# Optimization experiments

Measured on AMD Instinct MI355X. Metric: run time of the kernel, lower is better.

Reference implementation:

```python
import jax, jax.numpy as jnp
import numpy as np

DIM = 384
DSTATE = 16
DTRANK = 24  # ceil(384/16)
DCONV = 3
F = 3  # fixed segment factor from rearrange 'b (f t) c'


def setup_inputs() -> dict:
    key = jax.random.key(0)
    ks = jax.random.split(key, 8)
    d_in = DIM // 2
    x = jax.random.normal(ks[0], (4, 6144, DIM), dtype=jnp.float32)
    in_proj_w = jax.random.normal(ks[1], (DIM, DIM), dtype=jnp.float32) * 0.05
    in_proj_b = jnp.zeros((DIM,), jnp.float32)
    conv_w = jax.random.normal(ks[2], (d_in, 2, DCONV), dtype=jnp.float32) * 0.3
    conv_b = jnp.zeros((d_in,), jnp.float32)
    A = jnp.tile(jnp.arange(1, DSTATE + 1, dtype=jnp.float32)[None, :], (d_in, 1))
    A_log = jnp.log(A)
    Ab_log = jnp.log(A)
    D = jnp.ones((d_in,), jnp.float32)
    x_proj_w = jax.random.normal(ks[3], (DTRANK + 2 * DSTATE, d_in), dtype=jnp.float32) * 0.05
    dt_init_std = DTRANK ** (-0.5)
    dt_proj_w = jax.random.uniform(ks[4], (d_in, DTRANK), minval=-dt_init_std, maxval=dt_init_std, dtype=jnp.float32)
    dt = jnp.exp(jax.random.uniform(ks[5], (d_in,), dtype=jnp.float32) * (np.log(0.1) - np.log(0.001)) + np.log(0.001))
    dt = jnp.clip(dt, 1e-4)
    dt_proj_b = dt + jnp.log(-jnp.expm1(-dt))
    out_proj_w = jax.random.normal(ks[6], (DIM, DIM), dtype=jnp.float32) * 0.05
    out_proj_b = jnp.zeros((DIM,), jnp.float32)
    return dict(x=x, in_proj_w=in_proj_w, in_proj_b=in_proj_b, conv_w=conv_w, conv_b=conv_b,
                A_log=A_log, Ab_log=Ab_log, D=D, x_proj_w=x_proj_w, dt_proj_w=dt_proj_w,
                dt_proj_b=dt_proj_b, out_proj_w=out_proj_w, out_proj_b=out_proj_b)


def _ssm(u, Amat, x_proj_w, dt_proj_w, dt_proj_b, Dvec):
    # u: (b, d, l) selective scan (no z-gating; z handled outside by concat)
    x_dbl = jnp.einsum('rd,bdl->brl', x_proj_w, u)
    dt = x_dbl[:, :DTRANK]                      # (b, r, l)
    Bm = x_dbl[:, DTRANK:DTRANK + DSTATE]       # (b, n, l)
    Cm = x_dbl[:, DTRANK + DSTATE:]             # (b, n, l)
    delta = jax.nn.softplus(jnp.einsum('dr,brl->bdl', dt_proj_w, dt) + dt_proj_b[None, :, None])
    dA = jnp.exp(jnp.einsum('bdl,dn->lbdn', delta, Amat))      # (l, b, d, n)
    dBu = jnp.einsum('bdl,bnl->lbdn', delta * u, Bm)           # (l, b, d, n)
    Ct = jnp.transpose(Cm, (2, 0, 1))                          # (l, b, n)
    h0 = jnp.zeros(u.shape[:2] + (DSTATE,), u.dtype)

    def step(h, inp):
        dA_t, dBu_t, C_t = inp
        h = dA_t * h + dBu_t
        return h, jnp.einsum('bdn,bn->bd', h, C_t)

    _, ys = jax.lax.scan(step, h0, (dA, dBu, Ct))
    return jnp.transpose(ys, (1, 2, 0)) + u * Dvec[None, :, None]


def reference(x, in_proj_w, in_proj_b, conv_w, conv_b, A_log, Ab_log, D,
              x_proj_w, dt_proj_w, dt_proj_b, out_proj_w, out_proj_b):
    b, seqlen, dim = x.shape
    t = seqlen // F
    xp = (x @ in_proj_w.T + in_proj_b).reshape(b * F, t, dim)
    xp = jnp.transpose(xp, (0, 2, 1))  # (bf, dim, t)
    xc = jax.lax.conv_general_dilated(xp, conv_w, (1,), 'SAME',
                                      dimension_numbers=('NCH', 'OIH', 'NCH'),
                                      feature_group_count=dim // 2)
    xc = jax.nn.silu(xc + conv_b[None, :, None])  # (bf, dim//2, t)
    z = xc
    A = -jnp.exp(A_log)
    Ab = -jnp.exp(Ab_log)
    fwd = _ssm(xc, A, x_proj_w, dt_proj_w, dt_proj_b, D)
    bwd = jnp.flip(_ssm(jnp.flip(xc, -1), Ab, x_proj_w, dt_proj_w, dt_proj_b, D), -1)
    y = jnp.concatenate([fwd + bwd, z], axis=1)   # (bf, dim, t)
    y = jnp.transpose(y, (0, 2, 1))
    out = y @ out_proj_w.T + out_proj_b
    return out.reshape(b, seqlen, dim)
```

## Files before the change

### kernel.cpp

```cpp
#include <hip/hip_runtime.h>
#include <hip/hip_bf16.h>
#include <math.h>

#define NSQ   12
#define LQ    2048
#define DIMQ  384
#define DIQ   192
#define RKQ   24
#define NCHK  16
#define CLEN  128

#define BM 128
#define BN 64
#define BK 64

typedef unsigned short u16;
typedef __attribute__((ext_vector_type(8))) short s16x8;
typedef __attribute__((ext_vector_type(4))) float f32x4;
typedef __attribute__((ext_vector_type(4))) unsigned short u16x4;
typedef __attribute__((ext_vector_type(8))) unsigned short u16x8;

__device__ __forceinline__ float siluf(float x) {
  return x / (1.0f + __expf(-x));
}
__device__ __forceinline__ float softplusf(float x) {
  return (x > 20.0f) ? x : log1pf(expf(x));
}
__device__ __forceinline__ u16 f2bf(float f) {
  unsigned int u = __float_as_uint(f);
  u += 0x7FFFu + ((u >> 16) & 1u);
  return (u16)(u >> 16);
}
__device__ __forceinline__ float bf2f(u16 h) {
  return __uint_as_float(((unsigned int)h) << 16);
}

union F4 { float4 v; float a[4]; };

template<int CTRL>
__device__ __forceinline__ float dpp_add(float x) {
  union { float f; int i; } u, r;
  u.f = x;
  r.i = __builtin_amdgcn_update_dpp(0, u.i, CTRL, 0xF, 0xF, true);
  return x + r.f;
}

__global__ void k_prep(const float* __restrict__ xpw, const float* __restrict__ dtw,
                       const float* __restrict__ inw, const float* __restrict__ outw,
                       u16* __restrict__ winb, u16* __restrict__ woutb,
                       u16* __restrict__ wc_hi, u16* __restrict__ wc_lo) {
  int t = threadIdx.x + blockIdx.x * blockDim.x;
  int stride = blockDim.x * gridDim.x;
  for (int i = t; i < DIMQ * DIMQ; i += stride) {
    winb[i]  = f2bf(inw[i]);
    woutb[i] = f2bf(outw[i]);
  }
  for (int i = t; i < 224 * 192; i += stride) {
    const int r = i / 192, k = i % 192;
    float v;
    if (r < 192) {
      float s = 0.0f;
      for (int q = 0; q < RKQ; ++q) s = fmaf(dtw[r * RKQ + q], xpw[q * 192 + k], s);
      v = s;
    } else {
      v = xpw[(24 + (r - 192)) * 192 + k];
    }
    const u16 hi = f2bf(v);
    wc_hi[i] = hi;
    wc_lo[i] = f2bf(v - bf2f(hi));
  }
}

__launch_bounds__(256)
__global__ void k_inproj(const float* __restrict__ x, const u16* __restrict__ wbf,
                         const float* __restrict__ bias, float* __restrict__ xp_t) {
  __shared__ __align__(16) char smem[33792];
  u16 (*As)[72] = (u16(*)[72])smem;
  u16 (*Bs)[72] = (u16(*)[72])(smem + 18432);
  const int t = threadIdx.x;
  const int m0 = blockIdx.x * BM;
  const int n0 = blockIdx.y * BN;
  const int lane = t & 63, wid = t >> 6;
  const int wm = wid >> 1, wn = wid & 1;
  const int lr = lane & 15, lg = lane >> 4;
  f32x4 acc[4][2];
#pragma unroll
  for (int i = 0; i < 4; ++i)
#pragma unroll
    for (int j = 0; j < 2; ++j) acc[i][j] = (f32x4){0.f, 0.f, 0.f, 0.f};

  for (int k0 = 0; k0 < 384; k0 += BK) {
    float4 a_ld[8];
#pragma unroll
    for (int i = 0; i < 8; ++i) {
      const int idx = t + i * 256;
      const int row = idx >> 4, kq = (idx & 15) * 4;
      a_ld[i] = *(const float4*)&x[(size_t)(m0 + row) * 384 + k0 + kq];
    }
    u16x8 b_ld[2];
#pragma unroll
    for (int i = 0; i < 2; ++i) {
      const int idx = t + i * 256;
      const int n = idx >> 3, kq = (idx & 7) * 8;
      b_ld[i] = *(const u16x8*)&wbf[(size_t)(n0 + n) * 384 + k0 + kq];
    }
    __syncthreads();
#pragma unroll
    for (int i = 0; i < 8; ++i) {
      const int idx = t + i * 256;
      const int row = idx >> 4, kq = (idx & 15) * 4;
      u16x4 p;
      p.x = f2bf(a_ld[i].x); p.y = f2bf(a_ld[i].y);
      p.z = f2bf(a_ld[i].z); p.w = f2bf(a_ld[i].w);
      *(u16x4*)&As[row][kq] = p;
    }
#pragma unroll
    for (int i = 0; i < 2; ++i) {
      const int idx = t + i * 256;
      const int n = idx >> 3, kq = (idx & 7) * 8;
      *(u16x8*)&Bs[n][kq] = b_ld[i];
    }
    __syncthreads();
#pragma unroll
    for (int kh = 0; kh < BK; kh += 32) {
      s16x8 af[4], bf[2];
#pragma unroll
      for (int mi = 0; mi < 4; ++mi)
        af[mi] = *(const s16x8*)&As[wm * 64 + mi * 16 + lr][kh + lg * 8];
#pragma unroll
      for (int ni = 0; ni < 2; ++ni)
        bf[ni] = *(const s16x8*)&Bs[wn * 32 + ni * 16 + lr][kh + lg * 8];
#pragma unroll
      for (int mi = 0; mi < 4; ++mi)
#pragma unroll
        for (int ni = 0; ni < 2; ++ni)
          acc[mi][ni] = __builtin_amdgcn_mfma_f32_16x16x32_bf16(af[mi], bf[ni], acc[mi][ni], 0, 0, 0);
    }
    __syncthreads();
  }
  float (*T)[132] = (float(*)[132])smem;
#pragma unroll
  for (int mi = 0; mi < 4; ++mi)
#pragma unroll
    for (int ni = 0; ni < 2; ++ni) {
      const int c_loc = wn * 32 + ni * 16 + lr;
      const int m_loc = wm * 64 + mi * 16 + lg * 4;
      *(f32x4*)&T[c_loc][m_loc] = acc[mi][ni];
    }
  __syncthreads();
  const int s = m0 >> 11, p0 = m0 & 2047;
#pragma unroll
  for (int i = 0; i < 8; ++i) {
    const int idx = t + i * 256;
    const int c = idx >> 5, pq = (idx & 31) * 4;
    float4 v = *(const float4*)&T[c][pq];
    const float bv = bias[n0 + c];
    v.x += bv; v.y += bv; v.z += bv; v.w += bv;
    *(float4*)&xp_t[((size_t)s * 384 + n0 + c) * 2048 + p0 + pq] = v;
  }
}

__global__ void k_conv(const float* __restrict__ xp_t, const float* __restrict__ cw,
                       const float* __restrict__ cb, float* __restrict__ xc) {
  const int idx = blockIdx.x * 256 + threadIdx.x;
  const int p = idx & 2047;
  const int sd = idx >> 11;
  const int d = sd % DIQ, s = sd / DIQ;
  const float* r0 = &xp_t[((size_t)s * 384 + 2 * d) * 2048];
  const float* r1 = r0 + 2048;
  const float w00 = cw[d * 6 + 0], w01 = cw[d * 6 + 1], w02 = cw[d * 6 + 2];
  const float w10 = cw[d * 6 + 3], w11 = cw[d * 6 + 4], w12 = cw[d * 6 + 5];
  float acc = cb[d];
  if (p > 0)    acc += w00 * r0[p - 1] + w10 * r1[p - 1];
  acc += w01 * r0[p] + w11 * r1[p];
  if (p < 2047) acc += w02 * r0[p + 1] + w12 * r1[p + 1];
  xc[idx] = siluf(acc);
}

__launch_bounds__(256)
__global__ void k_xproj(const float* __restrict__ xc, const u16* __restrict__ wc_hi,
                        const u16* __restrict__ wc_lo, const float* __restrict__ dtb,
                        float* __restrict__ delta, float* __restrict__ bc) {
  __shared__ u16 Ah[224][40];
  __shared__ u16 Al[224][40];
  __shared__ u16 Bh[64][40];
  __shared__ u16 Bl[64][40];
  const int t = threadIdx.x;
  const int lane = t & 63, w = t >> 6;
  const int ln = lane & 15, lg = lane >> 4;
  const int blk = blockIdx.x;
  const int s = blk >> 5, l0 = (blk & 31) * 64;
  f32x4 acc[14];
#pragma unroll
  for (int mi = 0; mi < 14; ++mi) acc[mi] = (f32x4){0.f, 0.f, 0.f, 0.f};

  for (int kc = 0; kc < 192; kc += 32) {
    u16x8 wah[4], wal[4];
#pragma unroll
    for (int i = 0; i < 4; ++i) {
      const int idx = t + i * 256;
      if (idx < 896) {
        const int r = idx >> 2, kg = (idx & 3) * 8;
        wah[i] = *(const u16x8*)&wc_hi[(size_t)r * 192 + kc + kg];
        wal[i] = *(const u16x8*)&wc_lo[(size_t)r * 192 + kc + kg];
      }
    }
    float4 uld[2];
#pragma unroll
    for (int i = 0; i < 2; ++i) {
      const int idx = t + i * 256;
      const int k = idx >> 4, lq = (idx & 15) * 4;
      uld[i] = *(const float4*)&xc[((size_t)s * 192 + kc + k) * 2048 + l0 + lq];
    }
    __syncthreads();
#pragma unroll
    for (int i = 0; i < 4; ++i) {
      const int idx = t + i * 256;
      if (idx < 896) {
        const int r = idx >> 2, kg = (idx & 3) * 8;
        *(u16x8*)&Ah[r][kg] = wah[i];
        *(u16x8*)&Al[r][kg] = wal[i];
      }
    }
#pragma unroll
    for (int i = 0; i < 2; ++i) {
      const int idx = t + i * 256;
      const int k = idx >> 4, lq = (idx & 15) * 4;
      F4 v; v.v = uld[i];
#pragma unroll
      for (int j = 0; j < 4; ++j) {
        const float f = v.a[j];
        const u16 hi = f2bf(f);
        Bh[lq + j][k] = hi;
        Bl[lq + j][k] = f2bf(f - bf2f(hi));
      }
    }
    __syncthreads();
    const s16x8 bh = *(const s16x8*)&Bh[w * 16 + ln][lg * 8];
    const s16x8 bl = *(const s16x8*)&Bl[w * 16 + ln][lg * 8];
#pragma unroll
    for (int mi = 0; mi < 14; ++mi) {
      const s16x8 ah = *(const s16x8*)&Ah[mi * 16 + ln][lg * 8];
      const s16x8 al = *(const s16x8*)&Al[mi * 16 + ln][lg * 8];
      acc[mi] = __builtin_amdgcn_mfma_f32_16x16x32_bf16(ah, bh, acc[mi], 0, 0, 0);
      acc[mi] = __builtin_amdgcn_mfma_f32_16x16x32_bf16(al, bh, acc[mi], 0, 0, 0);
      acc[mi] = __builtin_amdgcn_mfma_f32_16x16x32_bf16(ah, bl, acc[mi], 0, 0, 0);
    }
    __syncthreads();
  }
  const int l = l0 + w * 16 + ln;
#pragma unroll
  for (int mi = 0; mi < 12; ++mi) {
    const int r0 = mi * 16 + lg * 4;
#pragma unroll
    for (int j = 0; j < 4; ++j) {
      const int r = r0 + j;
      delta[((size_t)s * 192 + r) * 2048 + l] = softplusf(acc[mi][j] + dtb[r]);
    }
  }
#pragma unroll
  for (int mi = 12; mi < 14; ++mi) {
    const int rr = (mi - 12) * 16 + lg * 4;
    float4 v;
    v.x = acc[mi][0]; v.y = acc[mi][1]; v.z = acc[mi][2]; v.w = acc[mi][3];
    *(float4*)&bc[((size_t)s * 2048 + l) * 32 + rr] = v;
  }
}

template<int DIR>
__launch_bounds__(256)
__global__ void k_scanA(const float* __restrict__ delta, const float* __restrict__ xc,
                        const float* __restrict__ bc, const float* __restrict__ A_log,
                        const float* __restrict__ Ab_log,
                        float* __restrict__ G, float* __restrict__ hc) {
  __shared__ float dch[16][132];
  __shared__ float uch[16][132];
  __shared__ float bsn[16][132];
  const int t = threadIdx.x;
  const int dl = t >> 4, n = t & 15;
  const int dg = blockIdx.x;
  const int s  = blockIdx.y;
  const int tc = blockIdx.z;
  const int d = dg * 16 + dl;
  const int base_l = DIR ? (LQ - CLEN * (tc + 1)) : (CLEN * tc);
  const float a = -__expf((DIR ? Ab_log : A_log)[d * 16 + n]);

  const size_t rb = ((size_t)s * 192 + dg * 16) * 2048 + base_l;
#pragma unroll
  for (int it = 0; it < 2; ++it) {
    const int i = t + it * 256;
    const int row = i >> 5, c4 = (i & 31) * 4;
    *(float4*)&dch[row][c4] = *(const float4*)&delta[rb + (size_t)row * 2048 + c4];
    *(float4*)&uch[row][c4] = *(const float4*)&xc[rb + (size_t)row * 2048 + c4];
  }
  const size_t bb = ((size_t)s * 2048 + base_l) * 32;
#pragma unroll
  for (int it = 0; it < 2; ++it) {
    const int i = t + it * 256;
    const int l = i >> 2, nq = (i & 3) * 4;
    F4 v; v.v = *(const float4*)&bc[bb + (size_t)l * 32 + nq];
#pragma unroll
    for (int k = 0; k < 4; ++k) bsn[nq + k][l] = v.a[k];
  }
  __syncthreads();
  float h = 0.0f, S = 0.0f;
#pragma unroll 4
  for (int qx = 0; qx < 32; ++qx) {
    const int q = DIR ? (31 - qx) : qx;
    const int lq = q * 4;
    F4 d4, u4, b4;
    d4.v = *(const float4*)&dch[dl][lq];
    u4.v = *(const float4*)&uch[dl][lq];
    b4.v = *(const float4*)&bsn[n][lq];
#pragma unroll
    for (int jj = 0; jj < 4; ++jj) {
      const int j = DIR ? (3 - jj) : jj;
      const float dlt = d4.a[j];
      const float dA = __expf(a * dlt);
      h = fmaf(dA, h, dlt * u4.a[j] * b4.a[j]);
      S += dlt;
    }
  }
  const size_t idx = (((size_t)(s * 2 + DIR) * NCHK + tc) * 192 + d) * 16 + n;
  G[idx] = __expf(a * S);
  hc[idx] = h;
}

__global__ void k_scanB(const float* __restrict__ G, float* __restrict__ hc) {
  const int gid = blockIdx.x * 256 + threadIdx.x;
  const int sd2 = gid / 3072;
  const int dn = gid % 3072;
  float h = 0.0f;
#pragma unroll
  for (int tc = 0; tc < NCHK; ++tc) {
    const size_t idx = ((size_t)sd2 * NCHK + tc) * 3072 + dn;
    const float g = G[idx];
    const float he = hc[idx];
    hc[idx] = h;
    h = fmaf(g, h, he);
  }
}

template<int DIR>
__launch_bounds__(256)
__global__ void k_scanC(const float* __restrict__ delta, const float* __restrict__ xc,
                        const float* __restrict__ bc, const float* __restrict__ A_log,
                        const float* __restrict__ Ab_log, const float* __restrict__ hc,
                        float* __restrict__ yf, float* __restrict__ yb) {
  __shared__ float dch[16][132];
  __shared__ float uch[16][132];
  __shared__ float bsn[16][132];
  __shared__ float csn[16][132];
  const int t = threadIdx.x;
  const int dl = t >> 4, n = t & 15;
  const int dg = blockIdx.x;
  const int s  = blockIdx.y;
  const int tc = blockIdx.z;
  const int d = dg * 16 + dl;
  const int base_l = DIR ? (LQ - CLEN * (tc + 1)) : (CLEN * tc);
  const float a = -__expf((DIR ? Ab_log : A_log)[d * 16 + n]);

  const size_t rb = ((size_t)s * 192 + dg * 16) * 2048 + base_l;
#pragma unroll
  for (int it = 0; it < 2; ++it) {
    const int i = t + it * 256;
    const int row = i >> 5, c4 = (i & 31) * 4;
    *(float4*)&dch[row][c4] = *(const float4*)&delta[rb + (size_t)row * 2048 + c4];
    *(float4*)&uch[row][c4] = *(const float4*)&xc[rb + (size_t)row * 2048 + c4];
  }
  const size_t bb = ((size_t)s * 2048 + base_l) * 32;
#pragma unroll
  for (int it = 0; it < 4; ++it) {
    const int i = t + it * 256;
    const int l = i >> 3, cq = (i & 7) * 4;
    F4 v; v.v = *(const float4*)&bc[bb + (size_t)l * 32 + cq];
    if (cq < 16) {
#pragma unroll
      for (int k = 0; k < 4; ++k) bsn[cq + k][l] = v.a[k];
    } else {
#pragma unroll
      for (int k = 0; k < 4; ++k) csn[cq - 16 + k][l] = v.a[k];
    }
  }
  const size_t idx = (((size_t)(s * 2 + DIR) * NCHK + tc) * 192 + d) * 16 + n;
  float h = hc[idx];
  __syncthreads();
  float* yrow = &(DIR ? yb : yf)[((size_t)s * 192 + d) * 2048 + base_l];
#pragma unroll 2
  for (int ww = 0; ww < 8; ++ww) {
    const int w = DIR ? (7 - ww) : ww;
    float ykeep = 0.0f;
#pragma unroll
    for (int qq = 0; qq < 4; ++qq) {
      const int q = DIR ? (3 - qq) : qq;
      const int lq = w * 16 + q * 4;
      F4 d4, u4, b4, c4;
      d4.v = *(const float4*)&dch[dl][lq];
      u4.v = *(const float4*)&uch[dl][lq];
      b4.v = *(const float4*)&bsn[n][lq];
      c4.v = *(const float4*)&csn[n][lq];
#pragma unroll
      for (int jj = 0; jj < 4; ++jj) {
        const int j = DIR ? (3 - jj) : jj;
        const float dlt = d4.a[j];
        const float dA = __expf(a * dlt);
        h = fmaf(dA, h, dlt * u4.a[j] * b4.a[j]);
        float yv = h * c4.a[j];
        yv = dpp_add<0x128>(yv);
        yv = dpp_add<0x124>(yv);
        yv = dpp_add<0x122>(yv);
        yv = dpp_add<0x121>(yv);
        ykeep = (q * 4 + j == n) ? yv : ykeep;
      }
    }
    yrow[w * 16 + n] = ykeep;
  }
}

#define SWC(l) (((l >> 2) & 7) << 3)
__launch_bounds__(256)
__global__ void k_combine(const float* __restrict__ yf, const float* __restrict__ yb,
                          const float* __restrict__ xc, const float* __restrict__ Dvec,
                          u16* __restrict__ Abuf) {
  __shared__ u16 T[64][72];
  const int t = threadIdx.x;
  const int cg = blockIdx.x;
  const int s  = blockIdx.y;
  const int l0 = blockIdx.z * 64;
  const int c0 = (cg < 3 ? cg : cg - 3) * 64;
#pragma unroll
  for (int i = 0; i < 4; ++i) {
    const int idx = t + i * 256;
    const int cr = idx >> 4, lq = (idx & 15) * 4;
    const size_t off = ((size_t)s * 192 + c0 + cr) * 2048 + l0 + lq;
    F4 v;
    if (cg < 3) {
      F4 f, g, u;
      f.v = *(const float4*)&yf[off];
      g.v = *(const float4*)&yb[off];
      u.v = *(const float4*)&xc[off];
      const float dv2 = 2.0f * Dvec[c0 + cr];
#pragma unroll
      for (int j = 0; j < 4; ++j) v.a[j] = f.a[j] + g.a[j] + dv2 * u.a[j];
    } else {
      v.v = *(const float4*)&xc[off];
    }
#pragma unroll
    for (int j = 0; j < 4; ++j) {
      const int l = lq + j;
      T[l][cr ^ SWC(l)] = f2bf(v.a[j]);
    }
  }
  __syncthreads();
  const int ccol = (cg < 3) ? cg * 64 : 192 + (cg - 3) * 64;
#pragma unroll
  for (int i = 0; i < 2; ++i) {
    const int idx = t + i * 256;
    const int l = idx >> 3, cq = (idx & 7) * 8;
    const u16x8 v = *(const u16x8*)&T[l][cq ^ SWC(l)];
    *(u16x8*)&Abuf[((size_t)s * 2048 + l0 + l) * 384 + ccol + cq] = v;
  }
}

__launch_bounds__(256)
__global__ void k_outproj(const u16* __restrict__ Abuf, const u16* __restrict__ wbf,
                          const float* __restrict__ bias, float* __restrict__ out) {
  __shared__ __align__(16) char smem[34816];
  u16 (*As)[72] = (u16(*)[72])smem;
  u16 (*Bs)[72] = (u16(*)[72])(smem + 18432);
  const int t = threadIdx.x;
  const int m0 = blockIdx.x * BM;
  const int n0 = blockIdx.y * BN;
  const int lane = t & 63, wid = t >> 6;
  const int wm = wid >> 1, wn = wid & 1;
  const int lr = lane & 15, lg = lane >> 4;
  f32x4 acc[4][2];
#pragma unroll
  for (int i = 0; i < 4; ++i)
#pragma unroll
    for (int j = 0; j < 2; ++j) acc[i][j] = (f32x4){0.f, 0.f, 0.f, 0.f};

  for (int k0 = 0; k0 < 384; k0 += BK) {
    u16x8 a_ld[4];
#pragma unroll
    for (int i = 0; i < 4; ++i) {
      const int idx = t + i * 256;
      const int row = idx >> 3, kq = (idx & 7) * 8;
      a_ld[i] = *(const u16x8*)&Abuf[(size_t)(m0 + row) * 384 + k0 + kq];
    }
    u16x8 b_ld[2];
#pragma unroll
    for (int i = 0; i < 2; ++i) {
      const int idx = t + i * 256;
      const int n = idx >> 3, kq = (idx & 7) * 8;
      b_ld[i] = *(const u16x8*)&wbf[(size_t)(n0 + n) * 384 + k0 + kq];
    }
    __syncthreads();
#pragma unroll
    for (int i = 0; i < 4; ++i) {
      const int idx = t + i * 256;
      const int row = idx >> 3, kq = (idx & 7) * 8;
      *(u16x8*)&As[row][kq] = a_ld[i];
    }
#pragma unroll
    for (int i = 0; i < 2; ++i) {
      const int idx = t + i * 256;
      const int n = idx >> 3, kq = (idx & 7) * 8;
      *(u16x8*)&Bs[n][kq] = b_ld[i];
    }
    __syncthreads();
#pragma unroll
    for (int kh = 0; kh < BK; kh += 32) {
      s16x8 af[4], bf[2];
#pragma unroll
      for (int mi = 0; mi < 4; ++mi)
        af[mi] = *(const s16x8*)&As[wm * 64 + mi * 16 + lr][kh + lg * 8];
#pragma unroll
      for (int ni = 0; ni < 2; ++ni)
        bf[ni] = *(const s16x8*)&Bs[wn * 32 + ni * 16 + lr][kh + lg * 8];
#pragma unroll
      for (int mi = 0; mi < 4; ++mi)
#pragma unroll
        for (int ni = 0; ni < 2; ++ni)
          acc[mi][ni] = __builtin_amdgcn_mfma_f32_16x16x32_bf16(af[mi], bf[ni], acc[mi][ni], 0, 0, 0);
    }
    __syncthreads();
  }
  float (*T)[68] = (float(*)[68])smem;
#pragma unroll
  for (int mi = 0; mi < 4; ++mi)
#pragma unroll
    for (int ni = 0; ni < 2; ++ni) {
      const int c_loc = wn * 32 + ni * 16 + lr;
      const int m_loc = wm * 64 + mi * 16 + lg * 4;
#pragma unroll
      for (int r = 0; r < 4; ++r) T[m_loc + r][c_loc] = acc[mi][ni][r];
    }
  __syncthreads();
#pragma unroll
  for (int i = 0; i < 8; ++i) {
    const int idx = t + i * 256;
    const int m = idx >> 4, cq = (idx & 15) * 4;
    float4 v = *(const float4*)&T[m][cq];
    const float4 bb = *(const float4*)&bias[n0 + cq];
    v.x += bb.x; v.y += bb.y; v.z += bb.z; v.w += bb.w;
    *(float4*)&out[(size_t)(m0 + m) * 384 + n0 + cq] = v;
  }
}

extern "C" void kernel_launch(void* const* d_in, const int* in_sizes, int n_in,
                              void* d_out, int out_size, void* d_ws, size_t ws_size,
                              hipStream_t stream) {
  const float* x     = (const float*)d_in[0];
  const float* inw   = (const float*)d_in[1];
  const float* inb   = (const float*)d_in[2];
  const float* convw = (const float*)d_in[3];
  const float* convb = (const float*)d_in[4];
  const float* alog  = (const float*)d_in[5];
  const float* ablog = (const float*)d_in[6];
  const float* Dv    = (const float*)d_in[7];
  const float* xpw   = (const float*)d_in[8];
  const float* dtw   = (const float*)d_in[9];
  const float* dtb   = (const float*)d_in[10];
  const float* outw  = (const float*)d_in[11];
  const float* outb  = (const float*)d_in[12];
  float* out = (float*)d_out;

  float* ws = (float*)d_ws;
  float* xp_t  = ws;
  float* xc    = xp_t + 9437184;
  float* delta = xc + 4718592;
  float* bc    = delta + 4718592;
  float* G     = bc + 786432;
  float* hc    = G + 1179648;
  u16*   winb  = (u16*)(hc + 1179648);
  u16*   woutb = winb + 147456;
  u16*   wc_hi = woutb + 147456;
  u16*   wc_lo = wc_hi + 43008;
  float* yf = xp_t;
  float* yb = xp_t + 4718592;
  u16*   Abuf = (u16*)delta;

  hipLaunchKernelGGL(k_prep,      dim3(96),         dim3(256), 0, stream, xpw, dtw, inw, outw, winb, woutb, wc_hi, wc_lo);
  hipLaunchKernelGGL(k_inproj,    dim3(192, 6),     dim3(256), 0, stream, x, winb, inb, xp_t);
  hipLaunchKernelGGL(k_conv,      dim3(18432),      dim3(256), 0, stream, xp_t, convw, convb, xc);
  hipLaunchKernelGGL(k_xproj,     dim3(384),        dim3(256), 0, stream, xc, wc_hi, wc_lo, dtb, delta, bc);
  hipLaunchKernelGGL((k_scanA<0>),dim3(12, 12, 16), dim3(256), 0, stream, delta, xc, bc, alog, ablog, G, hc);
  hipLaunchKernelGGL((k_scanA<1>),dim3(12, 12, 16), dim3(256), 0, stream, delta, xc, bc, alog, ablog, G, hc);
  hipLaunchKernelGGL(k_scanB,     dim3(288),        dim3(256), 0, stream, G, hc);
  hipLaunchKernelGGL((k_scanC<0>),dim3(12, 12, 16), dim3(256), 0, stream, delta, xc, bc, alog, ablog, hc, yf, yb);
  hipLaunchKernelGGL((k_scanC<1>),dim3(12, 12, 16), dim3(256), 0, stream, delta, xc, bc, alog, ablog, hc, yf, yb);
  hipLaunchKernelGGL(k_combine,   dim3(6, 12, 32),  dim3(256), 0, stream, yf, yb, xc, Dv, Abuf);
  hipLaunchKernelGGL(k_outproj,   dim3(192, 6),     dim3(256), 0, stream, Abuf, woutb, outb, out);
}
```

Baseline: 347.5 us.

## Fuse chunked scan passes into one kernel with decoupled look-back

Replaces the three-pass chunked scan (chunk-local scan, carry propagation, rescan with outputs) with a single kernel per direction. Blocks take chunk indices in order from an atomic ticket counter, publish each chunk's decay and end state with release flags, and spin on the flags of earlier chunks to build their incoming state before producing outputs. This removes two kernel launches per direction and the second load of delta, u and B/C from global memory, at the cost of spin-waiting, serialized look-back and a bounded-spin fallback that could yield wrong results if a flag never arrives.

```diff
diff --git a/kernel.cpp b/kernel.cpp
--- a/kernel.cpp
+++ b/kernel.cpp
@@ -69,6 +69,11 @@
     wc_hi[i] = hi;
     wc_lo[i] = f2bf(v - bf2f(hi));
   }
+}
+
+__global__ void k_init(int* __restrict__ sync) {
+  const int i = blockIdx.x * 256 + threadIdx.x;
+  if (i < 64 + 4608) sync[i] = 0;
 }
 
 __launch_bounds__(256)
@@ -269,18 +274,24 @@
 
 template<int DIR>
 __launch_bounds__(256)
-__global__ void k_scanA(const float* __restrict__ delta, const float* __restrict__ xc,
-                        const float* __restrict__ bc, const float* __restrict__ A_log,
-                        const float* __restrict__ Ab_log,
-                        float* __restrict__ G, float* __restrict__ hc) {
+__global__ void k_scan_fused(const float* __restrict__ delta, const float* __restrict__ xc,
+                             const float* __restrict__ bc, const float* __restrict__ A_log,
+                             const float* __restrict__ Ab_log,
+                             float* __restrict__ Gp, float* __restrict__ Hp,
+                             int* sync, float* __restrict__ yout) {
   __shared__ float dch[16][132];
   __shared__ float uch[16][132];
   __shared__ float bsn[16][132];
+  __shared__ float csn[16][132];
+  __shared__ int s_v;
   const int t = threadIdx.x;
+  if (t == 0) s_v = atomicAdd(&sync[DIR], 1);
+  __syncthreads();
+  const int v = s_v;
+  const int chain = v % 144;
+  const int tc = v / 144;
+  const int dg = chain % 12, s = chain / 12;
   const int dl = t >> 4, n = t & 15;
-  const int dg = blockIdx.x;
-  const int s  = blockIdx.y;
-  const int tc = blockIdx.z;
   const int d = dg * 16 + dl;
   const int base_l = DIR ? (LQ - CLEN * (tc + 1)) : (CLEN * tc);
   const float a = -__expf((DIR ? Ab_log : A_log)[d * 16 + n]);
@@ -295,14 +306,20 @@
   }
   const size_t bb = ((size_t)s * 2048 + base_l) * 32;
 #pragma unroll
-  for (int it = 0; it < 2; ++it) {
+  for (int it = 0; it < 4; ++it) {
     const int i = t + it * 256;
-    const int l = i >> 2, nq = (i & 3) * 4;
-    F4 v; v.v = *(const float4*)&bc[bb + (size_t)l * 32 + nq];
-#pragma unroll
-    for (int k = 0; k < 4; ++k) bsn[nq + k][l] = v.a[k];
+    const int l = i >> 3, cq = (i & 7) * 4;
+    F4 vv; vv.v = *(const float4*)&bc[bb + (size_t)l * 32 + cq];
+    if (cq < 16) {
+#pragma unroll
+      for (int k = 0; k < 4; ++k) bsn[cq + k][l] = vv.a[k];
+    } else {
+#pragma unroll
+      for (int k = 0; k < 4; ++k) csn[cq - 16 + k][l] = vv.a[k];
+    }
   }
   __syncthreads();
+
   float h = 0.0f, S = 0.0f;
 #pragma unroll 4
   for (int qx = 0; qx < 32; ++qx) {
@@ -316,76 +333,47 @@
     for (int jj = 0; jj < 4; ++jj) {
       const int j = DIR ? (3 - jj) : jj;
       const float dlt = d4.a[j];
-      const float dA = __expf(a * dlt);
-      h = fmaf(dA, h, dlt * u4.a[j] * b4.a[j]);
+      h = fmaf(__expf(a * dlt), h, dlt * u4.a[j] * b4.a[j]);
       S += dlt;
     }
   }
-  const size_t idx = (((size_t)(s * 2 + DIR) * NCHK + tc) * 192 + d) * 16 + n;
-  G[idx] = __expf(a * S);
-  hc[idx] = h;
-}
-
-__global__ void k_scanB(const float* __restrict__ G, float* __restrict__ hc) {
-  const int gid = blockIdx.x * 256 + threadIdx.x;
-  const int sd2 = gid / 3072;
-  const int dn = gid % 3072;
-  float h = 0.0f;
-#pragma unroll
-  for (int tc = 0; tc < NCHK; ++tc) {
-    const size_t idx = ((size_t)sd2 * NCHK + tc) * 3072 + dn;
-    const float g = G[idx];
-    const float he = hc[idx];
-    hc[idx] = h;
-    h = fmaf(g, h, he);
-  }
-}
-
-template<int DIR>
-__launch_bounds__(256)
-__global__ void k_scanC(const float* __restrict__ delta, const float* __restrict__ xc,
-                        const float* __restrict__ bc, const float* __restrict__ A_log,
-                        const float* __restrict__ Ab_log, const float* __restrict__ hc,
-                        float* __restrict__ yf, float* __restrict__ yb) {
-  __shared__ float dch[16][132];
-  __shared__ float uch[16][132];
-  __shared__ float bsn[16][132];
-  __shared__ float csn[16][132];
-  const int t = threadIdx.x;
-  const int dl = t >> 4, n = t & 15;
-  const int dg = blockIdx.x;
-  const int s  = blockIdx.y;
-  const int tc = blockIdx.z;
-  const int d = dg * 16 + dl;
-  const int base_l = DIR ? (LQ - CLEN * (tc + 1)) : (CLEN * tc);
-  const float a = -__expf((DIR ? Ab_log : A_log)[d * 16 + n]);
-
-  const size_t rb = ((size_t)s * 192 + dg * 16) * 2048 + base_l;
-#pragma unroll
-  for (int it = 0; it < 2; ++it) {
-    const int i = t + it * 256;
-    const int row = i >> 5, c4 = (i & 31) * 4;
-    *(float4*)&dch[row][c4] = *(const float4*)&delta[rb + (size_t)row * 2048 + c4];
-    *(float4*)&uch[row][c4] = *(const float4*)&xc[rb + (size_t)row * 2048 + c4];
-  }
-  const size_t bb = ((size_t)s * 2048 + base_l) * 32;
-#pragma unroll
-  for (int it = 0; it < 4; ++it) {
-    const int i = t + it * 256;
-    const int l = i >> 3, cq = (i & 7) * 4;
-    F4 v; v.v = *(const float4*)&bc[bb + (size_t)l * 32 + cq];
-    if (cq < 16) {
-#pragma unroll
-      for (int k = 0; k < 4; ++k) bsn[cq + k][l] = v.a[k];
-    } else {
-#pragma unroll
-      for (int k = 0; k < 4; ++k) csn[cq - 16 + k][l] = v.a[k];
-    }
-  }
-  const size_t idx = (((size_t)(s * 2 + DIR) * NCHK + tc) * 192 + d) * 16 + n;
-  float h = hc[idx];
-  __syncthreads();
-  float* yrow = &(DIR ? yb : yf)[((size_t)s * 192 + d) * 2048 + base_l];
+  const float Gv = __expf(a * S);
+
+  int* flags = sync + 64;
+  const int sbase = (DIR * 144 + chain) * NCHK;
+  if (tc < NCHK - 1) {
+    Gp[(size_t)(sbase + tc) * 256 + t] = Gv;
+    Hp[(size_t)(sbase + tc) * 256 + t] = h;
+    __threadfence();
+    __syncthreads();
+    if (t == 0)
+      __hip_atomic_store(&flags[sbase + tc], 1, __ATOMIC_RELEASE, __HIP_MEMORY_SCOPE_AGENT);
+  }
+
+  float hin = 0.0f;
+  if (tc > 0) {
+    float mult = 1.0f, carry = 0.0f;
+    for (int p = tc - 1; p >= 0; --p) {
+      const int ps = sbase + p;
+      if (t == 0) {
+        int cnt = 0;
+        while (__hip_atomic_load(&flags[ps], __ATOMIC_ACQUIRE, __HIP_MEMORY_SCOPE_AGENT) == 0) {
+          if (++cnt > (1 << 24)) break;
+        }
+      }
+      __syncthreads();
+      const int hb = __hip_atomic_load((const int*)&Hp[(size_t)ps * 256 + t],
+                                       __ATOMIC_RELAXED, __HIP_MEMORY_SCOPE_AGENT);
+      const int gb = __hip_atomic_load((const int*)&Gp[(size_t)ps * 256 + t],
+                                       __ATOMIC_RELAXED, __HIP_MEMORY_SCOPE_AGENT);
+      carry = fmaf(mult, __int_as_float(hb), carry);
+      mult *= __int_as_float(gb);
+    }
+    hin = carry;
+  }
+
+  h = hin;
+  float* yrow = &yout[((size_t)s * 192 + d) * 2048 + base_l];
 #pragma unroll 2
   for (int ww = 0; ww < 8; ++ww) {
     const int w = DIR ? (7 - ww) : ww;
@@ -403,8 +391,7 @@
       for (int jj = 0; jj < 4; ++jj) {
         const int j = DIR ? (3 - jj) : jj;
         const float dlt = d4.a[j];
-        const float dA = __expf(a * dlt);
-        h = fmaf(dA, h, dlt * u4.a[j] * b4.a[j]);
+        h = fmaf(__expf(a * dlt), h, dlt * u4.a[j] * b4.a[j]);
         float yv = h * c4.a[j];
         yv = dpp_add<0x128>(yv);
         yv = dpp_add<0x124>(yv);
@@ -577,19 +564,18 @@
   u16*   woutb = winb + 147456;
   u16*   wc_hi = woutb + 147456;
   u16*   wc_lo = wc_hi + 43008;
+  int*   sync  = (int*)(wc_lo + 43008);
   float* yf = xp_t;
   float* yb = xp_t + 4718592;
   u16*   Abuf = (u16*)delta;
 
-  hipLaunchKernelGGL(k_prep,      dim3(96),         dim3(256), 0, stream, xpw, dtw, inw, outw, winb, woutb, wc_hi, wc_lo);
-  hipLaunchKernelGGL(k_inproj,    dim3(192, 6),     dim3(256), 0, stream, x, winb, inb, xp_t);
-  hipLaunchKernelGGL(k_conv,      dim3(18432),      dim3(256), 0, stream, xp_t, convw, convb, xc);
-  hipLaunchKernelGGL(k_xproj,     dim3(384),        dim3(256), 0, stream, xc, wc_hi, wc_lo, dtb, delta, bc);
-  hipLaunchKernelGGL((k_scanA<0>),dim3(12, 12, 16), dim3(256), 0, stream, delta, xc, bc, alog, ablog, G, hc);
-  hipLaunchKernelGGL((k_scanA<1>),dim3(12, 12, 16), dim3(256), 0, stream, delta, xc, bc, alog, ablog, G, hc);
-  hipLaunchKernelGGL(k_scanB,     dim3(288),        dim3(256), 0, stream, G, hc);
-  hipLaunchKernelGGL((k_scanC<0>),dim3(12, 12, 16), dim3(256), 0, stream, delta, xc, bc, alog, ablog, hc, yf, yb);
-  hipLaunchKernelGGL((k_scanC<1>),dim3(12, 12, 16), dim3(256), 0, stream, delta, xc, bc, alog, ablog, hc, yf, yb);
-  hipLaunchKernelGGL(k_combine,   dim3(6, 12, 32),  dim3(256), 0, stream, yf, yb, xc, Dv, Abuf);
-  hipLaunchKernelGGL(k_outproj,   dim3(192, 6),     dim3(256), 0, stream, Abuf, woutb, outb, out);
-}
+  hipLaunchKernelGGL(k_prep,         dim3(96),        dim3(256), 0, stream, xpw, dtw, inw, outw, winb, woutb, wc_hi, wc_lo);
+  hipLaunchKernelGGL(k_init,         dim3(19),        dim3(256), 0, stream, sync);
+  hipLaunchKernelGGL(k_inproj,       dim3(192, 6),    dim3(256), 0, stream, x, winb, inb, xp_t);
+  hipLaunchKernelGGL(k_conv,         dim3(18432),     dim3(256), 0, stream, xp_t, convw, convb, xc);
+  hipLaunchKernelGGL(k_xproj,        dim3(384),       dim3(256), 0, stream, xc, wc_hi, wc_lo, dtb, delta, bc);
+  hipLaunchKernelGGL((k_scan_fused<0>), dim3(2304),   dim3(256), 0, stream, delta, xc, bc, alog, ablog, G, hc, sync, yf);
+  hipLaunchKernelGGL((k_scan_fused<1>), dim3(2304),   dim3(256), 0, stream, delta, xc, bc, alog, ablog, G, hc, sync, yb);
+  hipLaunchKernelGGL(k_combine,      dim3(6, 12, 32), dim3(256), 0, stream, yf, yb, xc, Dv, Abuf);
+  hipLaunchKernelGGL(k_outproj,      dim3(192, 6),    dim3(256), 0, stream, Abuf, woutb, outb, out);
+}
```

Measured after the change: 1.035 ms. +197.8%, slower.

## Fuse forward and backward scan passes per chunk; prefetch GEMM tiles into registers

Applied to the files above, without the earlier changes.

The scanA and scanC kernels now handle both directions in one block. Each block loads a chunk's delta, u, B and C once into shared memory and runs the forward and the reversed recurrences interleaved, which halves chunk loads and kernel launches and gives two independent dependency chains for ILP. Backward chunk indices are remapped so the scanB carry layout stays unchanged. The in-projection and out-projection GEMMs now issue the next k-tile's global loads into registers before the MFMA loop and drop one barrier per iteration. The cost is higher register pressure in the fused scan kernels, which may lower occupancy.

```diff
diff --git a/kernel.cpp b/kernel.cpp
--- a/kernel.cpp
+++ b/kernel.cpp
@@ -83,44 +83,39 @@
   const int lane = t & 63, wid = t >> 6;
   const int wm = wid >> 1, wn = wid & 1;
   const int lr = lane & 15, lg = lane >> 4;
+  const int ar0 = t >> 4, akq = (t & 15) * 4;
+  const int br0 = t >> 3, bkq = (t & 7) * 8;
   f32x4 acc[4][2];
 #pragma unroll
   for (int i = 0; i < 4; ++i)
 #pragma unroll
     for (int j = 0; j < 2; ++j) acc[i][j] = (f32x4){0.f, 0.f, 0.f, 0.f};
 
-  for (int k0 = 0; k0 < 384; k0 += BK) {
-    float4 a_ld[8];
+  float4 a_ld[8];
+  u16x8 b_ld[2];
+#define IN_LOAD(KC) { \
+  _Pragma("unroll") \
+  for (int i = 0; i < 8; ++i) \
+    a_ld[i] = *(const float4*)&x[(size_t)(m0 + ar0 + i * 16) * 384 + (KC) * BK + akq]; \
+  _Pragma("unroll") \
+  for (int i = 0; i < 2; ++i) \
+    b_ld[i] = *(const u16x8*)&wbf[(size_t)(n0 + br0 + i * 32) * 384 + (KC) * BK + bkq]; \
+}
+  IN_LOAD(0);
+  for (int kc = 0; kc < 6; ++kc) {
+    __syncthreads();
 #pragma unroll
     for (int i = 0; i < 8; ++i) {
-      const int idx = t + i * 256;
-      const int row = idx >> 4, kq = (idx & 15) * 4;
-      a_ld[i] = *(const float4*)&x[(size_t)(m0 + row) * 384 + k0 + kq];
-    }
-    u16x8 b_ld[2];
-#pragma unroll
-    for (int i = 0; i < 2; ++i) {
-      const int idx = t + i * 256;
-      const int n = idx >> 3, kq = (idx & 7) * 8;
-      b_ld[i] = *(const u16x8*)&wbf[(size_t)(n0 + n) * 384 + k0 + kq];
-    }
-    __syncthreads();
-#pragma unroll
-    for (int i = 0; i < 8; ++i) {
-      const int idx = t + i * 256;
-      const int row = idx >> 4, kq = (idx & 15) * 4;
       u16x4 p;
       p.x = f2bf(a_ld[i].x); p.y = f2bf(a_ld[i].y);
       p.z = f2bf(a_ld[i].z); p.w = f2bf(a_ld[i].w);
-      *(u16x4*)&As[row][kq] = p;
-    }
-#pragma unroll
-    for (int i = 0; i < 2; ++i) {
-      const int idx = t + i * 256;
-      const int n = idx >> 3, kq = (idx & 7) * 8;
-      *(u16x8*)&Bs[n][kq] = b_ld[i];
-    }
+      *(u16x4*)&As[ar0 + i * 16][akq] = p;
+    }
+#pragma unroll
+    for (int i = 0; i < 2; ++i)
+      *(u16x8*)&Bs[br0 + i * 32][bkq] = b_ld[i];
     __syncthreads();
+    if (kc < 5) IN_LOAD(kc + 1);
 #pragma unroll
     for (int kh = 0; kh < BK; kh += 32) {
       s16x8 af[4], bf[2];
@@ -136,8 +131,9 @@
         for (int ni = 0; ni < 2; ++ni)
           acc[mi][ni] = __builtin_amdgcn_mfma_f32_16x16x32_bf16(af[mi], bf[ni], acc[mi][ni], 0, 0, 0);
     }
-    __syncthreads();
-  }
+  }
+#undef IN_LOAD
+  __syncthreads();
   float (*T)[132] = (float(*)[132])smem;
 #pragma unroll
   for (int mi = 0; mi < 4; ++mi)
@@ -267,7 +263,6 @@
   }
 }
 
-template<int DIR>
 __launch_bounds__(256)
 __global__ void k_scanA(const float* __restrict__ delta, const float* __restrict__ xc,
                         const float* __restrict__ bc, const float* __restrict__ A_log,
@@ -280,10 +275,11 @@
   const int dl = t >> 4, n = t & 15;
   const int dg = blockIdx.x;
   const int s  = blockIdx.y;
-  const int tc = blockIdx.z;
+  const int tcp = blockIdx.z;
   const int d = dg * 16 + dl;
-  const int base_l = DIR ? (LQ - CLEN * (tc + 1)) : (CLEN * tc);
-  const float a = -__expf((DIR ? Ab_log : A_log)[d * 16 + n]);
+  const int base_l = CLEN * tcp;
+  const float af = -__expf(A_log[d * 16 + n]);
+  const float ab = -__expf(Ab_log[d * 16 + n]);
 
   const size_t rb = ((size_t)s * 192 + dg * 16) * 2048 + base_l;
 #pragma unroll
@@ -303,27 +299,33 @@
     for (int k = 0; k < 4; ++k) bsn[nq + k][l] = v.a[k];
   }
   __syncthreads();
-  float h = 0.0f, S = 0.0f;
+  float hf = 0.0f, hb = 0.0f, S = 0.0f;
 #pragma unroll 4
   for (int qx = 0; qx < 32; ++qx) {
-    const int q = DIR ? (31 - qx) : qx;
-    const int lq = q * 4;
-    F4 d4, u4, b4;
-    d4.v = *(const float4*)&dch[dl][lq];
-    u4.v = *(const float4*)&uch[dl][lq];
-    b4.v = *(const float4*)&bsn[n][lq];
+    const int lqf = qx * 4;
+    const int lqb = (31 - qx) * 4;
+    F4 d4f, u4f, b4f, d4b, u4b, b4b;
+    d4f.v = *(const float4*)&dch[dl][lqf];
+    u4f.v = *(const float4*)&uch[dl][lqf];
+    b4f.v = *(const float4*)&bsn[n][lqf];
+    d4b.v = *(const float4*)&dch[dl][lqb];
+    u4b.v = *(const float4*)&uch[dl][lqb];
+    b4b.v = *(const float4*)&bsn[n][lqb];
 #pragma unroll
     for (int jj = 0; jj < 4; ++jj) {
-      const int j = DIR ? (3 - jj) : jj;
-      const float dlt = d4.a[j];
-      const float dA = __expf(a * dlt);
-      h = fmaf(dA, h, dlt * u4.a[j] * b4.a[j]);
-      S += dlt;
-    }
-  }
-  const size_t idx = (((size_t)(s * 2 + DIR) * NCHK + tc) * 192 + d) * 16 + n;
-  G[idx] = __expf(a * S);
-  hc[idx] = h;
+      { const float dlt = d4f.a[jj];
+        hf = fmaf(__expf(af * dlt), hf, dlt * u4f.a[jj] * b4f.a[jj]);
+        S += dlt; }
+      { const int j = 3 - jj;
+        const float dlt = d4b.a[j];
+        hb = fmaf(__expf(ab * dlt), hb, dlt * u4b.a[j] * b4b.a[j]); }
+    }
+  }
+  const int dn = d * 16 + n;
+  const size_t idx_f = ((size_t)(s * 2 + 0) * NCHK + tcp) * 3072 + dn;
+  const size_t idx_b = ((size_t)(s * 2 + 1) * NCHK + (NCHK - 1 - tcp)) * 3072 + dn;
+  G[idx_f] = __expf(af * S);  hc[idx_f] = hf;
+  G[idx_b] = __expf(ab * S);  hc[idx_b] = hb;
 }
 
 __global__ void k_scanB(const float* __restrict__ G, float* __restrict__ hc) {
@@ -341,7 +343,6 @@
   }
 }
 
-template<int DIR>
 __launch_bounds__(256)
 __global__ void k_scanC(const float* __restrict__ delta, const float* __restrict__ xc,
                         const float* __restrict__ bc, const float* __restrict__ A_log,
@@ -355,10 +356,11 @@
   const int dl = t >> 4, n = t & 15;
   const int dg = blockIdx.x;
   const int s  = blockIdx.y;
-  const int tc = blockIdx.z;
+  const int tcp = blockIdx.z;
   const int d = dg * 16 + dl;
-  const int base_l = DIR ? (LQ - CLEN * (tc + 1)) : (CLEN * tc);
-  const float a = -__expf((DIR ? Ab_log : A_log)[d * 16 + n]);
+  const int base_l = CLEN * tcp;
+  const float af = -__expf(A_log[d * 16 + n]);
+  const float ab = -__expf(Ab_log[d * 16 + n]);
 
   const size_t rb = ((size_t)s * 192 + dg * 16) * 2048 + base_l;
 #pragma unroll
@@ -382,38 +384,56 @@
       for (int k = 0; k < 4; ++k) csn[cq - 16 + k][l] = v.a[k];
     }
   }
-  const size_t idx = (((size_t)(s * 2 + DIR) * NCHK + tc) * 192 + d) * 16 + n;
-  float h = hc[idx];
+  const int dn = d * 16 + n;
+  const size_t idx_f = ((size_t)(s * 2 + 0) * NCHK + tcp) * 3072 + dn;
+  const size_t idx_b = ((size_t)(s * 2 + 1) * NCHK + (NCHK - 1 - tcp)) * 3072 + dn;
+  float hf = hc[idx_f];
+  float hb = hc[idx_b];
   __syncthreads();
-  float* yrow = &(DIR ? yb : yf)[((size_t)s * 192 + d) * 2048 + base_l];
+  float* yrf = &yf[((size_t)s * 192 + d) * 2048 + base_l];
+  float* yrb = &yb[((size_t)s * 192 + d) * 2048 + base_l];
 #pragma unroll 2
   for (int ww = 0; ww < 8; ++ww) {
-    const int w = DIR ? (7 - ww) : ww;
-    float ykeep = 0.0f;
+    const int wf = ww, wb = 7 - ww;
+    float ykf = 0.0f, ykb = 0.0f;
 #pragma unroll
     for (int qq = 0; qq < 4; ++qq) {
-      const int q = DIR ? (3 - qq) : qq;
-      const int lq = w * 16 + q * 4;
-      F4 d4, u4, b4, c4;
-      d4.v = *(const float4*)&dch[dl][lq];
-      u4.v = *(const float4*)&uch[dl][lq];
-      b4.v = *(const float4*)&bsn[n][lq];
-      c4.v = *(const float4*)&csn[n][lq];
+      const int qf = qq, qb = 3 - qq;
+      const int lqf = wf * 16 + qf * 4;
+      const int lqb = wb * 16 + qb * 4;
+      F4 d4f, u4f, b4f, c4f, d4b, u4b, b4b, c4b;
+      d4f.v = *(const float4*)&dch[dl][lqf];
+      u4f.v = *(const float4*)&uch[dl][lqf];
+      b4f.v = *(const float4*)&bsn[n][lqf];
+      c4f.v = *(const float4*)&csn[n][lqf];
+      d4b.v = *(const float4*)&dch[dl][lqb];
+      u4b.v = *(const float4*)&uch[dl][lqb];
+      b4b.v = *(const float4*)&bsn[n][lqb];
+      c4b.v = *(const float4*)&csn[n][lqb];
 #pragma unroll
       for (int jj = 0; jj < 4; ++jj) {
-        const int j = DIR ? (3 - jj) : jj;
-        const float dlt = d4.a[j];
-        const float dA = __expf(a * dlt);
-        h = fmaf(dA, h, dlt * u4.a[j] * b4.a[j]);
-        float yv = h * c4.a[j];
-        yv = dpp_add<0x128>(yv);
-        yv = dpp_add<0x124>(yv);
-        yv = dpp_add<0x122>(yv);
-        yv = dpp_add<0x121>(yv);
-        ykeep = (q * 4 + j == n) ? yv : ykeep;
+        { const int j = jj;
+          const float dlt = d4f.a[j];
+          hf = fmaf(__expf(af * dlt), hf, dlt * u4f.a[j] * b4f.a[j]);
+          float yv = hf * c4f.a[j];
+          yv = dpp_add<0x128>(yv);
+          yv = dpp_add<0x124>(yv);
+          yv = dpp_add<0x122>(yv);
+          yv = dpp_add<0x121>(yv);
+          ykf = (qf * 4 + j == n) ? yv : ykf; }
+        { const int j = 3 - jj;
+          const float dlt = d4b.a[j];
+          hb = fmaf(__expf(ab * dlt), hb, dlt * u4b.a[j] * b4b.a[j]);
+          float yv = hb * c4b.a[j];
+          yv = dpp_add<0x128>(yv);
+          yv = dpp_add<0x124>(yv);
+          yv = dpp_add<0x122>(yv);
+          yv = dpp_add<0x121>(yv);
+          ykb = (qb * 4 + j == n) ? yv : ykb; }
       }
     }
-    yrow[w * 16 + n] = ykeep;
+    yrf[wf * 16 + n] = ykf;
+    yrb[wb * 16 + n] = ykb;
   }
 }
 
@@ -474,41 +494,34 @@
   const int lane = t & 63, wid = t >> 6;
   const int wm = wid >> 1, wn = wid & 1;
   const int lr = lane & 15, lg = lane >> 4;
+  const int ar0 = t >> 3, akq = (t & 7) * 8;
+  const int br0 = t >> 3, bkq = (t & 7) * 8;
   f32x4 acc[4][2];
 #pragma unroll
   for (int i = 0; i < 4; ++i)
 #pragma unroll
     for (int j = 0; j < 2; ++j) acc[i][j] = (f32x4){0.f, 0.f, 0.f, 0.f};
 
-  for (int k0 = 0; k0 < 384; k0 += BK) {
-    u16x8 a_ld[4];
-#pragma unroll
-    for (int i = 0; i < 4; ++i) {
-      const int idx = t + i * 256;
-      const int row = idx >> 3, kq = (idx & 7) * 8;
-      a_ld[i] = *(const u16x8*)&Abuf[(size_t)(m0 + row) * 384 + k0 + kq];
-    }
-    u16x8 b_ld[2];
-#pragma unroll
-    for (int i = 0; i < 2; ++i) {
-      const int idx = t + i * 256;
-      const int n = idx >> 3, kq = (idx & 7) * 8;
-      b_ld[i] = *(const u16x8*)&wbf[(size_t)(n0 + n) * 384 + k0 + kq];
-    }
+  u16x8 a_ld[4], b_ld[2];
+#define OUT_LOAD(KC) { \
+  _Pragma("unroll") \
+  for (int i = 0; i < 4; ++i) \
+    a_ld[i] = *(const u16x8*)&Abuf[(size_t)(m0 + ar0 + i * 32) * 384 + (KC) * BK + akq]; \
+  _Pragma("unroll") \
+  for (int i = 0; i < 2; ++i) \
+    b_ld[i] = *(const u16x8*)&wbf[(size_t)(n0 + br0 + i * 32) * 384 + (KC) * BK + bkq]; \
+}
+  OUT_LOAD(0);
+  for (int kc = 0; kc < 6; ++kc) {
     __syncthreads();
 #pragma unroll
-    for (int i = 0; i < 4; ++i) {
-      const int idx = t + i * 256;
-      const int row = idx >> 3, kq = (idx & 7) * 8;
-      *(u16x8*)&As[row][kq] = a_ld[i];
-    }
-#pragma unroll
-    for (int i = 0; i < 2; ++i) {
-      const int idx = t + i * 256;
-      const int n = idx >> 3, kq = (idx & 7) * 8;
-      *(u16x8*)&Bs[n][kq] = b_ld[i];
-    }
+    for (int i = 0; i < 4; ++i)
+      *(u16x8*)&As[ar0 + i * 32][akq] = a_ld[i];
+#pragma unroll
+    for (int i = 0; i < 2; ++i)
+      *(u16x8*)&Bs[br0 + i * 32][bkq] = b_ld[i];
     __syncthreads();
+    if (kc < 5) OUT_LOAD(kc + 1);
 #pragma unroll
     for (int kh = 0; kh < BK; kh += 32) {
       s16x8 af[4], bf[2];
@@ -524,8 +537,9 @@
         for (int ni = 0; ni < 2; ++ni)
           acc[mi][ni] = __builtin_amdgcn_mfma_f32_16x16x32_bf16(af[mi], bf[ni], acc[mi][ni], 0, 0, 0);
     }
-    __syncthreads();
-  }
+  }
+#undef OUT_LOAD
+  __syncthreads();
   float (*T)[68] = (float(*)[68])smem;
 #pragma unroll
   for (int mi = 0; mi < 4; ++mi)
@@ -581,15 +595,13 @@
   float* yb = xp_t + 4718592;
   u16*   Abuf = (u16*)delta;
 
-  hipLaunchKernelGGL(k_prep,      dim3(96),         dim3(256), 0, stream, xpw, dtw, inw, outw, winb, woutb, wc_hi, wc_lo);
-  hipLaunchKernelGGL(k_inproj,    dim3(192, 6),     dim3(256), 0, stream, x, winb, inb, xp_t);
-  hipLaunchKernelGGL(k_conv,      dim3(18432),      dim3(256), 0, stream, xp_t, convw, convb, xc);
-  hipLaunchKernelGGL(k_xproj,     dim3(384),        dim3(256), 0, stream, xc, wc_hi, wc_lo, dtb, delta, bc);
-  hipLaunchKernelGGL((k_scanA<0>),dim3(12, 12, 16), dim3(256), 0, stream, delta, xc, bc, alog, ablog, G, hc);
-  hipLaunchKernelGGL((k_scanA<1>),dim3(12, 12, 16), dim3(256), 0, stream, delta, xc, bc, alog, ablog, G, hc);
-  hipLaunchKernelGGL(k_scanB,     dim3(288),        dim3(256), 0, stream, G, hc);
-  hipLaunchKernelGGL((k_scanC<0>),dim3(12, 12, 16), dim3(256), 0, stream, delta, xc, bc, alog, ablog, hc, yf, yb);
-  hipLaunchKernelGGL((k_scanC<1>),dim3(12, 12, 16), dim3(256), 0, stream, delta, xc, bc, alog, ablog, hc, yf, yb);
-  hipLaunchKernelGGL(k_combine,   dim3(6, 12, 32),  dim3(256), 0, stream, yf, yb, xc, Dv, Abuf);
-  hipLaunchKernelGGL(k_outproj,   dim3(192, 6),     dim3(256), 0, stream, Abuf, woutb, outb, out);
-}
+  hipLaunchKernelGGL(k_prep,    dim3(96),         dim3(256), 0, stream, xpw, dtw, inw, outw, winb, woutb, wc_hi, wc_lo);
+  hipLaunchKernelGGL(k_inproj,  dim3(192, 6),     dim3(256), 0, stream, x, winb, inb, xp_t);
+  hipLaunchKernelGGL(k_conv,    dim3(18432),      dim3(256), 0, stream, xp_t, convw, convb, xc);
+  hipLaunchKernelGGL(k_xproj,   dim3(384),        dim3(256), 0, stream, xc, wc_hi, wc_lo, dtb, delta, bc);
+  hipLaunchKernelGGL(k_scanA,   dim3(12, 12, 16), dim3(256), 0, stream, delta, xc, bc, alog, ablog, G, hc);
+  hipLaunchKernelGGL(k_scanB,   dim3(288),        dim3(256), 0, stream, G, hc);
+  hipLaunchKernelGGL(k_scanC,   dim3(12, 12, 16), dim3(256), 0, stream, delta, xc, bc, alog, ablog, hc, yf, yb);
+  hipLaunchKernelGGL(k_combine, dim3(6, 12, 32),  dim3(256), 0, stream, yf, yb, xc, Dv, Abuf);
+  hipLaunchKernelGGL(k_outproj, dim3(192, 6),     dim3(256), 0, stream, Abuf, woutb, outb, out);
+}
```

New measurement: 331.5 us. 1.05x faster.
